# Optimization experiments

Hardware: AMD Instinct MI355X
Metric: run time of the kernel (lower is better)

Reference implementation:

```python
import jax, jax.numpy as jnp
import numpy as np

N = 40000; E = 640000; F_IN = 128; HID = 32; HEADS = 4; G = 64
NEG_SLOPE = 0.2; LN_EPS = 1e-5


def setup_inputs() -> dict:
    key = jax.random.key(0)
    ks = jax.random.split(key, 24)
    rn = lambda k, shape, s=0.1: jax.random.normal(k, shape, jnp.float32) * s
    d = {}
    d["x"] = jax.random.normal(ks[0], (N, F_IN), jnp.float32)
    d["edge_index"] = jax.random.randint(ks[1], (2, E), 0, N)
    d["batch"] = jnp.sort(jax.random.randint(ks[2], (N,), 0, G))
    # GAT layer 0: in F_IN -> HID per head, HEADS heads, concat
    d["W0"] = rn(ks[3], (F_IN, HEADS * HID))
    d["as0"] = rn(ks[4], (HEADS, HID)); d["ad0"] = rn(ks[5], (HEADS, HID))
    d["b0"] = jnp.zeros((HEADS * HID,), jnp.float32)
    d["ln0_g"] = jnp.ones((HEADS * HID,), jnp.float32); d["ln0_b"] = jnp.zeros((HEADS * HID,), jnp.float32)
    # GAT layer 1: HEADS*HID -> HID per head, HEADS heads, concat
    d["W1"] = rn(ks[6], (HEADS * HID, HEADS * HID))
    d["as1"] = rn(ks[7], (HEADS, HID)); d["ad1"] = rn(ks[8], (HEADS, HID))
    d["b1"] = jnp.zeros((HEADS * HID,), jnp.float32)
    d["ln1_g"] = jnp.ones((HEADS * HID,), jnp.float32); d["ln1_b"] = jnp.zeros((HEADS * HID,), jnp.float32)
    # GAT layer 2: HEADS*HID -> HID, 1 head, no concat
    d["W2"] = rn(ks[9], (HEADS * HID, HID))
    d["as2"] = rn(ks[10], (1, HID)); d["ad2"] = rn(ks[11], (1, HID))
    d["b2"] = jnp.zeros((HID,), jnp.float32)
    d["ln2_g"] = jnp.ones((HID,), jnp.float32); d["ln2_b"] = jnp.zeros((HID,), jnp.float32)
    # classifier: HID -> HID//2 -> 2
    d["fc1_w"] = rn(ks[12], (HID, HID // 2)); d["fc1_b"] = jnp.zeros((HID // 2,), jnp.float32)
    d["fc2_w"] = rn(ks[13], (HID // 2, 2)); d["fc2_b"] = jnp.zeros((2,), jnp.float32)
    return d


def gat_layer(x, src, dst, W, a_s, a_d, b, heads, out_c, concat):
    n = x.shape[0]
    h = (x @ W).reshape(n, heads, out_c)            # [N,H,C]
    al_s = jnp.sum(h * a_s, axis=-1)                # [N,H]
    al_d = jnp.sum(h * a_d, axis=-1)                # [N,H]
    e = jax.nn.leaky_relu(al_s[src] + al_d[dst], NEG_SLOPE)  # [E,H]
    m = jax.ops.segment_max(e, dst, num_segments=n)          # segment softmax over dst
    ex = jnp.exp(e - m[dst])
    s = jax.ops.segment_sum(ex, dst, num_segments=n)
    alpha = ex / (s[dst] + 1e-16)                   # [E,H]
    out = jax.ops.segment_sum(h[src] * alpha[:, :, None], dst, num_segments=n)  # [N,H,C]
    out = out.reshape(n, heads * out_c) if concat else out.mean(axis=1)
    return out + b


def layer_norm(x, g, b):
    mu = x.mean(-1, keepdims=True)
    var = jnp.var(x, axis=-1, keepdims=True)
    return (x - mu) * jax.lax.rsqrt(var + LN_EPS) * g + b


def reference(x, edge_index, batch, W0, as0, ad0, b0, ln0_g, ln0_b, W1, as1, ad1, b1, ln1_g, ln1_b, W2, as2, ad2, b2, ln2_g, ln2_b, fc1_w, fc1_b, fc2_w, fc2_b):
    src, dst = edge_index[0], edge_index[1]
    h = gat_layer(x, src, dst, W0, as0, ad0, b0, HEADS, HID, True)
    h = jax.nn.elu(layer_norm(h, ln0_g, ln0_b))
    h = gat_layer(h, src, dst, W1, as1, ad1, b1, HEADS, HID, True)
    h = jax.nn.elu(layer_norm(h, ln1_g, ln1_b))
    h = gat_layer(h, src, dst, W2, as2, ad2, b2, 1, HID, False)
    h = jax.nn.elu(layer_norm(h, ln2_g, ln2_b))
    cnt = jax.ops.segment_sum(jnp.ones((h.shape[0],), h.dtype), batch, num_segments=G)
    hg = jax.ops.segment_sum(h, batch, num_segments=G) / jnp.maximum(cnt, 1.0)[:, None]  # global mean pool [G,HID]
    z = jax.nn.relu(hg @ fc1_w + fc1_b)
    return z @ fc2_w + fc2_b
```

## Files before the change

kernel.cpp:

```cpp
#include <hip/hip_runtime.h>
#include <hip/hip_fp16.h>
#include <math.h>

#define NN 40000
#define EE 640000
#define NG 64
#define SCAN_BLOCKS ((NN + 1023) / 1024)

__device__ __forceinline__ float eluf(float x) { return x > 0.f ? x : expm1f(x); }

typedef const __attribute__((address_space(1))) char gas_char;
typedef __attribute__((address_space(3))) char las_char;

__device__ __forceinline__ void async_copy16(void* l, const void* g) {
  __builtin_amdgcn_global_load_lds((gas_char*)g, (las_char*)l, 16, 0, 0);
}

typedef __fp16 f16x2 __attribute__((ext_vector_type(2)));
__device__ __forceinline__ unsigned packh(float lo, float hi) {
  f16x2 p = __builtin_amdgcn_cvt_pkrtz(lo, hi);
  union { f16x2 h; unsigned u; } c; c.h = p; return c.u;
}
__device__ __forceinline__ float hlo(unsigned p) {
  union { unsigned u; f16x2 h; } c; c.u = p; return (float)c.h.x;
}
__device__ __forceinline__ float hhi(unsigned p) {
  union { unsigned u; f16x2 h; } c; c.u = p; return (float)c.h.y;
}

__global__ void zero_int_kernel(int* __restrict__ p, int n) {
  int i = blockIdx.x * 256 + threadIdx.x;
  if (i < n) p[i] = 0;
}

__global__ void count_deg_kernel(const int* __restrict__ dst, int* __restrict__ deg, int e) {
  int i = blockIdx.x * 256 + threadIdx.x;
  if (i < e) atomicAdd(&deg[dst[i]], 1);
}

__global__ __launch_bounds__(1024) void scanA_kernel(const int* __restrict__ deg,
                                                     int* __restrict__ row_ptr,
                                                     int* __restrict__ bsum, int n) {
  __shared__ int wsum[16];
  int t = threadIdx.x, lane = t & 63, wid = t >> 6;
  int i = blockIdx.x * 1024 + t;
  int v = (i < n) ? deg[i] : 0;
#pragma unroll
  for (int off = 1; off < 64; off <<= 1) {
    int u = __shfl_up(v, off);
    if (lane >= off) v += u;
  }
  if (lane == 63) wsum[wid] = v;
  __syncthreads();
  if (t < 16) {
    int w = wsum[t];
#pragma unroll
    for (int off = 1; off < 16; off <<= 1) {
      int u = __shfl_up(w, off);
      if (t >= off) w += u;
    }
    wsum[t] = w;
  }
  __syncthreads();
  if (wid > 0) v += wsum[wid - 1];
  if (i < n) row_ptr[i + 1] = v;
  if (t == 1023) bsum[blockIdx.x] = v;
}

__global__ void scanB_kernel(const int* __restrict__ bsum, int* __restrict__ boff, int nb) {
  int lane = threadIdx.x;
  int v = (lane < nb) ? bsum[lane] : 0;
  int orig = v;
#pragma unroll
  for (int off = 1; off < 64; off <<= 1) {
    int u = __shfl_up(v, off);
    if (lane >= off) v += u;
  }
  if (lane < nb) boff[lane] = v - orig;
}

__global__ __launch_bounds__(1024) void scanC_kernel(int* __restrict__ row_ptr,
                                                     const int* __restrict__ boff,
                                                     int* __restrict__ cursor, int n) {
  int i = blockIdx.x * 1024 + threadIdx.x;
  if (i < n) {
    int v = row_ptr[i + 1] + boff[i >> 10];
    row_ptr[i + 1] = v;
    if (i + 1 < n) cursor[i + 1] = v;
    if (i == 0) { cursor[0] = 0; row_ptr[0] = 0; }
  }
}

__global__ void scatter_kernel(const int* __restrict__ src, const int* __restrict__ dst,
                               int* __restrict__ cursor, int* __restrict__ csr_src, int e) {
  int i = blockIdx.x * 256 + threadIdx.x;
  if (i < e) {
    int d = dst[i];
    int pos = atomicAdd(&cursor[d], 1);
    csr_src[pos] = src[i];
  }
}

__global__ __launch_bounds__(256, 3) void gemm128_kernel(
    const float* __restrict__ x, const float* __restrict__ W,
    const float* __restrict__ a_s, const float* __restrict__ a_d,
    unsigned* __restrict__ hb, float* __restrict__ als, float* __restrict__ ald)
{
  __shared__ float xs[2][64 * 32];
  __shared__ float ws[2][32 * 128];

  int t = threadIdx.x;
  int row0 = blockIdx.x * 64;
  const char* xgb = (const char*)x + (size_t)row0 * 512;

  {
    int li0 = t, li1 = t + 256;
    async_copy16((char*)xs[0] + li0 * 16, xgb + (li0 >> 3) * 512 + (li0 & 7) * 16);
    async_copy16((char*)xs[0] + li1 * 16, xgb + (li1 >> 3) * 512 + (li1 & 7) * 16);
    const char* wg = (const char*)W;
#pragma unroll
    for (int p = 0; p < 4; ++p)
      async_copy16((char*)ws[0] + p * 4096 + t * 16, wg + p * 4096 + t * 16);
  }
  __syncthreads();

  int cg = t & 31, rg = t >> 5;
  int r0 = rg * 8;
  int jlo = 2 * cg;

  float acc[8][4];
#pragma unroll
  for (int r = 0; r < 8; ++r)
#pragma unroll
    for (int c = 0; c < 4; ++c) acc[r][c] = 0.f;

  for (int ch = 0; ch < 4; ++ch) {
    if (ch < 3) {
      int b = (ch + 1) & 1;
      int li0 = t, li1 = t + 256;
      const char* xg = xgb + (ch + 1) * 128;
      async_copy16((char*)xs[b] + li0 * 16, xg + (li0 >> 3) * 512 + (li0 & 7) * 16);
      async_copy16((char*)xs[b] + li1 * 16, xg + (li1 >> 3) * 512 + (li1 & 7) * 16);
      const char* wg = (const char*)W + (size_t)(ch + 1) * 32 * 128 * 4;
#pragma unroll
      for (int p = 0; p < 4; ++p)
        async_copy16((char*)ws[b] + p * 4096 + t * 16, wg + p * 4096 + t * 16);
    }
    const float* wc = ws[ch & 1];
    const float* xc = xs[ch & 1];
#pragma unroll
    for (int kk = 0; kk < 32; kk += 4) {
      float2 wlo[4], whi[4];
#pragma unroll
      for (int q = 0; q < 4; ++q) {
        wlo[q] = *reinterpret_cast<const float2*>(&wc[(kk + q) * 128 + jlo]);
        whi[q] = *reinterpret_cast<const float2*>(&wc[(kk + q) * 128 + 64 + jlo]);
      }
#pragma unroll
      for (int r = 0; r < 8; ++r) {
        float4 xv = *reinterpret_cast<const float4*>(&xc[(r0 + r) * 32 + kk]);
        float a0 = acc[r][0], a1 = acc[r][1], a2 = acc[r][2], a3 = acc[r][3];
        a0 = fmaf(xv.x, wlo[0].x, a0); a1 = fmaf(xv.x, wlo[0].y, a1);
        a2 = fmaf(xv.x, whi[0].x, a2); a3 = fmaf(xv.x, whi[0].y, a3);
        a0 = fmaf(xv.y, wlo[1].x, a0); a1 = fmaf(xv.y, wlo[1].y, a1);
        a2 = fmaf(xv.y, whi[1].x, a2); a3 = fmaf(xv.y, whi[1].y, a3);
        a0 = fmaf(xv.z, wlo[2].x, a0); a1 = fmaf(xv.z, wlo[2].y, a1);
        a2 = fmaf(xv.z, whi[2].x, a2); a3 = fmaf(xv.z, whi[2].y, a3);
        a0 = fmaf(xv.w, wlo[3].x, a0); a1 = fmaf(xv.w, wlo[3].y, a1);
        a2 = fmaf(xv.w, whi[3].x, a2); a3 = fmaf(xv.w, whi[3].y, a3);
        acc[r][0] = a0; acc[r][1] = a1; acc[r][2] = a2; acc[r][3] = a3;
      }
    }
    __syncthreads();
  }

#pragma unroll
  for (int r = 0; r < 8; ++r) {
    uint2 pv;
    pv.x = packh(acc[r][0], acc[r][2]);
    pv.y = packh(acc[r][1], acc[r][3]);
    *reinterpret_cast<uint2*>(&hb[(size_t)(row0 + r0 + r) * 64 + jlo]) = pv;
  }

  float as0 = a_s[jlo], as1 = a_s[jlo + 1], as2 = a_s[jlo + 64], as3 = a_s[jlo + 65];
  float ad0 = a_d[jlo], ad1 = a_d[jlo + 1], ad2 = a_d[jlo + 64], ad3 = a_d[jlo + 65];
  int lane = t & 63;
#pragma unroll
  for (int r = 0; r < 8; ++r) {
    float psa = fmaf(acc[r][0], as0, acc[r][1] * as1);
    float psb = fmaf(acc[r][2], as2, acc[r][3] * as3);
    float pda = fmaf(acc[r][0], ad0, acc[r][1] * ad1);
    float pdb = fmaf(acc[r][2], ad2, acc[r][3] * ad3);
#pragma unroll
    for (int m = 1; m < 16; m <<= 1) {
      psa += __shfl_xor(psa, m); psb += __shfl_xor(psb, m);
      pda += __shfl_xor(pda, m); pdb += __shfl_xor(pdb, m);
    }
    if ((lane & 15) == 0) {
      int hA = (lane >> 4) & 1;
      size_t row = (size_t)(row0 + r0 + r);
      als[row * 4 + hA] = psa; als[row * 4 + hA + 2] = psb;
      ald[row * 4 + hA] = pda; ald[row * 4 + hA + 2] = pdb;
    }
  }
}

__global__ __launch_bounds__(256, 2) void gemm32_kernel(
    const float* __restrict__ x, const float* __restrict__ W,
    const float* __restrict__ a_s, const float* __restrict__ a_d,
    float* __restrict__ h, float* __restrict__ als, float* __restrict__ ald)
{
  __shared__ float xs[64 * 128];
  __shared__ float ws[2][32 * 32];
  int t = threadIdx.x;
  int row0 = blockIdx.x * 64;
  {
    const char* xg = (const char*)(x + (size_t)row0 * 128);
    char* xl = (char*)xs;
#pragma unroll
    for (int it = 0; it < 8; ++it)
      async_copy16(xl + it * 4096 + t * 16, xg + it * 4096 + t * 16);
  }
  async_copy16((char*)ws[0] + t * 16, (const char*)W + t * 16);
  __syncthreads();

  int cg = t & 7, rg = t >> 3;
  int r0 = rg * 2, c0 = cg * 4;
  float acc[2][4];
#pragma unroll
  for (int r = 0; r < 2; ++r)
#pragma unroll
    for (int c = 0; c < 4; ++c) acc[r][c] = 0.f;

  for (int ch = 0; ch < 4; ++ch) {
    if (ch < 3) {
      const char* wg = (const char*)W + (size_t)(ch + 1) * 32 * 32 * 4;
      async_copy16((char*)ws[(ch + 1) & 1] + t * 16, wg + t * 16);
    }
    const float* wc = ws[ch & 1];
    const float* xc = xs + ch * 32;
#pragma unroll
    for (int kk = 0; kk < 32; kk += 4) {
      float4 wv[4];
#pragma unroll
      for (int q = 0; q < 4; ++q)
        wv[q] = *reinterpret_cast<const float4*>(&wc[(kk + q) * 32 + c0]);
#pragma unroll
      for (int r = 0; r < 2; ++r) {
        float4 xv = *reinterpret_cast<const float4*>(&xc[(r0 + r) * 128 + kk]);
#pragma unroll
        for (int c = 0; c < 4; ++c) {
          float a = acc[r][c];
          a = fmaf(xv.x, (&wv[0].x)[c], a);
          a = fmaf(xv.y, (&wv[1].x)[c], a);
          a = fmaf(xv.z, (&wv[2].x)[c], a);
          a = fmaf(xv.w, (&wv[3].x)[c], a);
          acc[r][c] = a;
        }
      }
    }
    __syncthreads();
  }

#pragma unroll
  for (int r = 0; r < 2; ++r) {
    float4 hv = make_float4(acc[r][0], acc[r][1], acc[r][2], acc[r][3]);
    *reinterpret_cast<float4*>(&h[(size_t)(row0 + r0 + r) * 32 + c0]) = hv;
  }
  float asv[4], adv[4];
#pragma unroll
  for (int c = 0; c < 4; ++c) { asv[c] = a_s[c0 + c]; adv[c] = a_d[c0 + c]; }
#pragma unroll
  for (int r = 0; r < 2; ++r) {
    float ps = acc[r][0] * asv[0] + acc[r][1] * asv[1] + acc[r][2] * asv[2] + acc[r][3] * asv[3];
    float pd = acc[r][0] * adv[0] + acc[r][1] * adv[1] + acc[r][2] * adv[2] + acc[r][3] * adv[3];
#pragma unroll
    for (int m = 1; m < 8; m <<= 1) { ps += __shfl_xor(ps, m); pd += __shfl_xor(pd, m); }
    if ((t & 7) == 0) {
      als[row0 + r0 + r] = ps;
      ald[row0 + r0 + r] = pd;
    }
  }
}

__global__ __launch_bounds__(256) void aggregate128_kernel(
    const unsigned* __restrict__ hb, const float* __restrict__ als, const float* __restrict__ ald,
    const int* __restrict__ row_ptr, const int* __restrict__ csr_src,
    const float* __restrict__ bias, const float* __restrict__ ln_g, const float* __restrict__ ln_b,
    float* __restrict__ out, int n)
{
  __shared__ int s_src[4][64];
  __shared__ float2 s_w[4][64][2];
  int t = threadIdx.x, lane = t & 63, wid = t >> 6;
  int node = blockIdx.x * 4 + wid;
  if (node >= n) return;
  int start = row_ptr[node], end = row_ptr[node + 1];
  int deg = end - start;

  float4 adq = reinterpret_cast<const float4*>(ald)[node];
  float adl[4] = {adq.x, adq.y, adq.z, adq.w};
  int hi = lane >> 5, c = lane & 31;
  int hsel = c >> 4;
  float a0 = 0.f, a1 = 0.f, a2 = 0.f, a3 = 0.f;
  float ssum0 = 0.f, ssum1 = 0.f;

  if (deg <= 64) {
    int s = 0;
    if (lane < deg) s = csr_src[start + lane];
    float4 q = reinterpret_cast<const float4*>(als)[s];
    float v[4] = {q.x, q.y, q.z, q.w};
    float ex[4];
#pragma unroll
    for (int hh = 0; hh < 4; ++hh) {
      float w = v[hh] + adl[hh];
      w = w > 0.f ? w : 0.2f * w;
      ex[hh] = __expf(w);
    }
    s_src[wid][lane] = s;
    s_w[wid][lane][0] = make_float2(ex[0], ex[2]);
    s_w[wid][lane][1] = make_float2(ex[1], ex[3]);

    int d1 = deg >> 1, d0c = deg - d1;
    int base = hi ? d0c : 0;
    int cnt = hi ? d1 : d0c;
    float b0a = 0.f, b1a = 0.f, b2a = 0.f, b3a = 0.f;
    float sb0 = 0.f, sb1 = 0.f;
    int j = 0;
    for (; j + 2 <= cnt; j += 2) {
      int sa = s_src[wid][base + j];
      int sb = s_src[wid][base + j + 1];
      uint2 ua = *reinterpret_cast<const uint2*>(&hb[(size_t)sa * 64 + 2 * c]);
      uint2 ub = *reinterpret_cast<const uint2*>(&hb[(size_t)sb * 64 + 2 * c]);
      float2 wa = s_w[wid][base + j][hsel];
      float2 wb = s_w[wid][base + j + 1][hsel];
      a0 = fmaf(wa.x, hlo(ua.x), a0); a1 = fmaf(wa.x, hlo(ua.y), a1);
      a2 = fmaf(wa.y, hhi(ua.x), a2); a3 = fmaf(wa.y, hhi(ua.y), a3);
      ssum0 += wa.x; ssum1 += wa.y;
      b0a = fmaf(wb.x, hlo(ub.x), b0a); b1a = fmaf(wb.x, hlo(ub.y), b1a);
      b2a = fmaf(wb.y, hhi(ub.x), b2a); b3a = fmaf(wb.y, hhi(ub.y), b3a);
      sb0 += wb.x; sb1 += wb.y;
    }
    if (j < cnt) {
      int sa = s_src[wid][base + j];
      uint2 ua = *reinterpret_cast<const uint2*>(&hb[(size_t)sa * 64 + 2 * c]);
      float2 wa = s_w[wid][base + j][hsel];
      a0 = fmaf(wa.x, hlo(ua.x), a0); a1 = fmaf(wa.x, hlo(ua.y), a1);
      a2 = fmaf(wa.y, hhi(ua.x), a2); a3 = fmaf(wa.y, hhi(ua.y), a3);
      ssum0 += wa.x; ssum1 += wa.y;
    }
    a0 += b0a; a1 += b1a; a2 += b2a; a3 += b3a;
    ssum0 += sb0; ssum1 += sb1;
    a0 += __shfl_xor(a0, 32); a1 += __shfl_xor(a1, 32);
    a2 += __shfl_xor(a2, 32); a3 += __shfl_xor(a3, 32);
    ssum0 += __shfl_xor(ssum0, 32); ssum1 += __shfl_xor(ssum1, 32);
  } else {
    for (int eb = start; eb < end; eb += 64) {
      int e = eb + lane;
      int s = 0;
      float exv[4] = {0.f, 0.f, 0.f, 0.f};
      if (e < end) {
        s = csr_src[e];
        float4 q = reinterpret_cast<const float4*>(als)[s];
        float av[4] = {q.x, q.y, q.z, q.w};
#pragma unroll
        for (int hh = 0; hh < 4; ++hh) {
          float v = av[hh] + adl[hh];
          v = v > 0.f ? v : 0.2f * v;
          exv[hh] = __expf(v);
        }
      }
      s_src[wid][lane] = s;
      s_w[wid][lane][0] = make_float2(exv[0], exv[2]);
      s_w[wid][lane][1] = make_float2(exv[1], exv[3]);
      int cnt = end - eb; if (cnt > 64) cnt = 64;
      for (int j = 0; j < cnt; ++j) {
        int sj = s_src[wid][j];
        uint2 u = *reinterpret_cast<const uint2*>(&hb[(size_t)sj * 64 + 2 * c]);
        float2 w = s_w[wid][j][hsel];
        a0 = fmaf(w.x, hlo(u.x), a0); a1 = fmaf(w.x, hlo(u.y), a1);
        a2 = fmaf(w.y, hhi(u.x), a2); a3 = fmaf(w.y, hhi(u.y), a3);
        ssum0 += w.x; ssum1 += w.y;
      }
    }
    a0 *= 0.5f; a1 *= 0.5f; a2 *= 0.5f; a3 *= 0.5f;
    ssum0 *= 0.5f; ssum1 *= 0.5f;
    a0 += __shfl_xor(a0, 32); a1 += __shfl_xor(a1, 32);
    a2 += __shfl_xor(a2, 32); a3 += __shfl_xor(a3, 32);
    ssum0 += __shfl_xor(ssum0, 32); ssum1 += __shfl_xor(ssum1, 32);
  }

  float2 blo = *reinterpret_cast<const float2*>(&bias[2 * c]);
  float2 bhi = *reinterpret_cast<const float2*>(&bias[2 * c + 64]);
  float is0 = 1.f / (ssum0 + 1e-16f), is1 = 1.f / (ssum1 + 1e-16f);
  float o0 = a0 * is0 + blo.x;
  float o1 = a1 * is0 + blo.y;
  float o2 = a2 * is1 + bhi.x;
  float o3 = a3 * is1 + bhi.y;
  float red = o0 + o1 + o2 + o3;
  float sq2 = o0 * o0 + o1 * o1 + o2 * o2 + o3 * o3;
#pragma unroll
  for (int m = 1; m < 64; m <<= 1) {
    red += __shfl_xor(red, m);
    sq2 += __shfl_xor(sq2, m);
  }
  float mu = red * (1.f / 256.f);
  float var = sq2 * (1.f / 256.f) - mu * mu;
  float rstd = rsqrtf(var + 1e-5f);
  int f = 2 * c + 64 * hi;
  float2 gv = *reinterpret_cast<const float2*>(&ln_g[f]);
  float2 bv = *reinterpret_cast<const float2*>(&ln_b[f]);
  float dx = (hi ? o2 : o0) - mu, dy = (hi ? o3 : o1) - mu;
  float2 yv;
  yv.x = eluf(dx * rstd * gv.x + bv.x);
  yv.y = eluf(dy * rstd * gv.y + bv.y);
  *reinterpret_cast<float2*>(&out[(size_t)node * 128 + f]) = yv;
}

__global__ __launch_bounds__(256) void aggregate32_kernel(
    const float* __restrict__ h, const float* __restrict__ als, const float* __restrict__ ald,
    const int* __restrict__ row_ptr, const int* __restrict__ csr_src,
    const float* __restrict__ bias, const float* __restrict__ ln_g, const float* __restrict__ ln_b,
    float* __restrict__ out, int n)
{
  __shared__ int s_src[4][64];
  __shared__ float s_ex[4][64];
  int t = threadIdx.x, lane = t & 63, wid = t >> 6;
  int node = blockIdx.x * 4 + wid;
  if (node >= n) return;
  int start = row_ptr[node], end = row_ptr[node + 1];
  int deg = end - start;
  float adl = ald[node];
  int hi = lane >> 5, col = lane & 31;
  float acc0 = 0.f, ssum = 0.f;

  if (deg <= 64) {
    int s = 0;
    if (lane < deg) s = csr_src[start + lane];
    float v = als[s] + adl;
    v = v > 0.f ? v : 0.2f * v;
    float ex = __expf(v);
    s_src[wid][lane] = s;
    s_ex[wid][lane] = ex;

    int d1 = deg >> 1, d0c = deg - d1;
    int base = hi ? d0c : 0;
    int cnt = hi ? d1 : d0c;
    float acc1 = 0.f, ssum1 = 0.f;
    int j = 0;
    for (; j + 2 <= cnt; j += 2) {
      int sa = s_src[wid][base + j];
      int sb = s_src[wid][base + j + 1];
      float ha = h[(size_t)sa * 32 + col];
      float hbv = h[(size_t)sb * 32 + col];
      float wa = s_ex[wid][base + j];
      float wb = s_ex[wid][base + j + 1];
      acc0 = fmaf(wa, ha, acc0); ssum += wa;
      acc1 = fmaf(wb, hbv, acc1); ssum1 += wb;
    }
    if (j < cnt) {
      float wa = s_ex[wid][base + j];
      acc0 = fmaf(wa, h[(size_t)s_src[wid][base + j] * 32 + col], acc0);
      ssum += wa;
    }
    acc0 += acc1; ssum += ssum1;
    acc0 += __shfl_xor(acc0, 32);
    ssum += __shfl_xor(ssum, 32);
  } else {
    for (int eb = start; eb < end; eb += 64) {
      int e = eb + lane;
      int s = 0; float ex = 0.f;
      if (e < end) {
        s = csr_src[e];
        float v = als[s] + adl;
        v = v > 0.f ? v : 0.2f * v;
        ex = __expf(v);
      }
      s_src[wid][lane] = s;
      s_ex[wid][lane] = ex;
      int cnt = end - eb; if (cnt > 64) cnt = 64;
      for (int j = 0; j < cnt; ++j) {
        float w = s_ex[wid][j];
        acc0 = fmaf(w, h[(size_t)s_src[wid][j] * 32 + col], acc0);
        ssum += w;
      }
    }
    acc0 *= 0.5f; ssum *= 0.5f;
    acc0 += __shfl_xor(acc0, 32);
    ssum += __shfl_xor(ssum, 32);
  }

  float o0 = acc0 / (ssum + 1e-16f) + bias[col];
  float red = o0, sq2 = o0 * o0;
#pragma unroll
  for (int m = 1; m < 64; m <<= 1) {
    red += __shfl_xor(red, m);
    sq2 += __shfl_xor(sq2, m);
  }
  float mu = red * (1.f / 64.f);
  float var = sq2 * (1.f / 64.f) - mu * mu;
  float rstd = rsqrtf(var + 1e-5f);
  float y0 = (o0 - mu) * rstd * ln_g[col] + ln_b[col];
  if (lane < 32) out[(size_t)node * 32 + col] = eluf(y0);
}

__device__ __forceinline__ int lower_bound_dev(const int* a, int n, int key) {
  int lo = 0, hi = n;
  while (lo < hi) { int mid = (lo + hi) >> 1; if (a[mid] < key) lo = mid + 1; else hi = mid; }
  return lo;
}

__global__ __launch_bounds__(256) void poolfc_kernel(
    const float* __restrict__ x2, const int* __restrict__ batch,
    const float* __restrict__ fc1w, const float* __restrict__ fc1b,
    const float* __restrict__ fc2w, const float* __restrict__ fc2b,
    float* __restrict__ out, int n)
{
  int g = blockIdx.x;
  int lo = lower_bound_dev(batch, n, g);
  int hi = lower_bound_dev(batch, n, g + 1);
  int t = threadIdx.x;
  int c = t & 31, r = t >> 5;
  float acc = 0.f;
  for (int i = lo + r; i < hi; i += 8) acc += x2[(size_t)i * 32 + c];
  __shared__ float red[8][32];
  __shared__ float hgl[32];
  __shared__ float zl[16];
  red[r][c] = acc;
  __syncthreads();
  if (r == 0) {
    float s = 0.f;
#pragma unroll
    for (int k = 0; k < 8; ++k) s += red[k][c];
    float cnt = (float)(hi - lo);
    hgl[c] = s / fmaxf(cnt, 1.f);
  }
  __syncthreads();
  if (t < 16) {
    float a = fc1b[t];
#pragma unroll
    for (int k = 0; k < 32; ++k) a = fmaf(hgl[k], fc1w[k * 16 + t], a);
    zl[t] = fmaxf(a, 0.f);
  }
  __syncthreads();
  if (t < 2) {
    float a = fc2b[t];
#pragma unroll
    for (int j = 0; j < 16; ++j) a = fmaf(zl[j], fc2w[j * 2 + t], a);
    out[g * 2 + t] = a;
  }
}

extern "C" void kernel_launch(void* const* d_in, const int* in_sizes, int n_in,
                              void* d_out, int out_size, void* d_ws, size_t ws_size,
                              hipStream_t stream) {
  const float* x    = (const float*)d_in[0];
  const int*   ei   = (const int*)d_in[1];
  const int*   batch= (const int*)d_in[2];
  const float* W0   = (const float*)d_in[3];
  const float* as0  = (const float*)d_in[4];
  const float* ad0  = (const float*)d_in[5];
  const float* b0   = (const float*)d_in[6];
  const float* ln0g = (const float*)d_in[7];
  const float* ln0b = (const float*)d_in[8];
  const float* W1   = (const float*)d_in[9];
  const float* as1  = (const float*)d_in[10];
  const float* ad1  = (const float*)d_in[11];
  const float* b1   = (const float*)d_in[12];
  const float* ln1g = (const float*)d_in[13];
  const float* ln1b = (const float*)d_in[14];
  const float* W2   = (const float*)d_in[15];
  const float* as2  = (const float*)d_in[16];
  const float* ad2  = (const float*)d_in[17];
  const float* b2   = (const float*)d_in[18];
  const float* ln2g = (const float*)d_in[19];
  const float* ln2b = (const float*)d_in[20];
  const float* fc1w = (const float*)d_in[21];
  const float* fc1b = (const float*)d_in[22];
  const float* fc2w = (const float*)d_in[23];
  const float* fc2b = (const float*)d_in[24];
  float* out = (float*)d_out;

  const int* srce = ei;
  const int* dste = ei + EE;

  unsigned* hb = (unsigned*)d_ws;
  float* B2  = (float*)(hb + (size_t)NN * 64);
  float* als = B2 + (size_t)NN * 128;
  float* ald = als + (size_t)NN * 4;
  float* h2  = ald + (size_t)NN * 4;
  float* x2  = h2 + (size_t)NN * 32;
  int* deg      = (int*)(x2 + (size_t)NN * 32);
  int* row_ptr  = deg + NN;
  int* cursor   = row_ptr + NN + 1;
  int* csr_src  = cursor + NN;
  int* bsum     = csr_src + EE;
  int* boff     = bsum + SCAN_BLOCKS;

  zero_int_kernel<<<(NN + 255) / 256, 256, 0, stream>>>(deg, NN);
  count_deg_kernel<<<(EE + 255) / 256, 256, 0, stream>>>(dste, deg, EE);
  scanA_kernel<<<SCAN_BLOCKS, 1024, 0, stream>>>(deg, row_ptr, bsum, NN);
  scanB_kernel<<<1, 64, 0, stream>>>(bsum, boff, SCAN_BLOCKS);
  scanC_kernel<<<SCAN_BLOCKS, 1024, 0, stream>>>(row_ptr, boff, cursor, NN);
  scatter_kernel<<<(EE + 255) / 256, 256, 0, stream>>>(srce, dste, cursor, csr_src, EE);

  gemm128_kernel<<<625, 256, 0, stream>>>(x, W0, as0, ad0, hb, als, ald);
  aggregate128_kernel<<<(NN + 3) / 4, 256, 0, stream>>>(hb, als, ald, row_ptr, csr_src,
                                                        b0, ln0g, ln0b, B2, NN);
  gemm128_kernel<<<625, 256, 0, stream>>>(B2, W1, as1, ad1, hb, als, ald);
  aggregate128_kernel<<<(NN + 3) / 4, 256, 0, stream>>>(hb, als, ald, row_ptr, csr_src,
                                                        b1, ln1g, ln1b, B2, NN);
  gemm32_kernel<<<625, 256, 0, stream>>>(B2, W2, as2, ad2, h2, als, ald);
  aggregate32_kernel<<<(NN + 3) / 4, 256, 0, stream>>>(h2, als, ald, row_ptr, csr_src,
                                                       b2, ln2g, ln2b, x2, NN);
  poolfc_kernel<<<NG, 256, 0, stream>>>(x2, batch, fc1w, fc1b, fc2w, fc2b, out, NN);
}
```

Before: 270.0 us.

## Assign one node per half-wavefront in aggregation and fuse scan block-offset pass

The aggregation kernels now map each node to a 32-lane half-wavefront instead of a full 64-lane wavefront, so each wave handles two nodes. Each half-wave processes all of its node's edges, which removes the cross-half shuffle reduction and shortens the layer-norm shuffle tree. The intent is better lane utilisation, since the average degree of about 16 left many lanes idle. Separately, the single-block scanB kernel is removed and each scanC block computes its own offset by summing the preceding block sums, saving one launch. The new launch grids rely on N being divisible by 8 and drop the node bounds check.

```diff
diff --git a/kernel.cpp b/kernel.cpp
--- a/kernel.cpp
+++ b/kernel.cpp
@@ -67,24 +67,23 @@
   if (t == 1023) bsum[blockIdx.x] = v;
 }
 
-__global__ void scanB_kernel(const int* __restrict__ bsum, int* __restrict__ boff, int nb) {
-  int lane = threadIdx.x;
-  int v = (lane < nb) ? bsum[lane] : 0;
-  int orig = v;
-#pragma unroll
-  for (int off = 1; off < 64; off <<= 1) {
-    int u = __shfl_up(v, off);
-    if (lane >= off) v += u;
-  }
-  if (lane < nb) boff[lane] = v - orig;
-}
-
 __global__ __launch_bounds__(1024) void scanC_kernel(int* __restrict__ row_ptr,
-                                                     const int* __restrict__ boff,
+                                                     const int* __restrict__ bsum,
                                                      int* __restrict__ cursor, int n) {
-  int i = blockIdx.x * 1024 + threadIdx.x;
+  __shared__ int off_s;
+  int t = threadIdx.x;
+  int b = blockIdx.x;
+  if (t < 64) {
+    int v = (t < b && t < SCAN_BLOCKS) ? bsum[t] : 0;
+#pragma unroll
+    for (int m = 1; m < 64; m <<= 1) v += __shfl_xor(v, m);
+    if (t == 0) off_s = v;
+  }
+  __syncthreads();
+  int off = off_s;
+  int i = b * 1024 + t;
   if (i < n) {
-    int v = row_ptr[i + 1] + boff[i >> 10];
+    int v = row_ptr[i + 1] + off;
     row_ptr[i + 1] = v;
     if (i + 1 < n) cursor[i + 1] = v;
     if (i == 0) { cursor[0] = 0; row_ptr[0] = 0; }
@@ -289,50 +288,44 @@
     const float* __restrict__ bias, const float* __restrict__ ln_g, const float* __restrict__ ln_b,
     float* __restrict__ out, int n)
 {
-  __shared__ int s_src[4][64];
-  __shared__ float2 s_w[4][64][2];
+  __shared__ int s_src[4][2][32];
+  __shared__ float2 s_w[4][2][32][2];
   int t = threadIdx.x, lane = t & 63, wid = t >> 6;
-  int node = blockIdx.x * 4 + wid;
-  if (node >= n) return;
+  int hw = lane >> 5, c = lane & 31;
+  int node = blockIdx.x * 8 + wid * 2 + hw;
   int start = row_ptr[node], end = row_ptr[node + 1];
   int deg = end - start;
 
   float4 adq = reinterpret_cast<const float4*>(ald)[node];
-  float adl[4] = {adq.x, adq.y, adq.z, adq.w};
-  int hi = lane >> 5, c = lane & 31;
   int hsel = c >> 4;
   float a0 = 0.f, a1 = 0.f, a2 = 0.f, a3 = 0.f;
   float ssum0 = 0.f, ssum1 = 0.f;
 
-  if (deg <= 64) {
+  if (deg <= 32) {
     int s = 0;
-    if (lane < deg) s = csr_src[start + lane];
-    float4 q = reinterpret_cast<const float4*>(als)[s];
-    float v[4] = {q.x, q.y, q.z, q.w};
-    float ex[4];
-#pragma unroll
-    for (int hh = 0; hh < 4; ++hh) {
-      float w = v[hh] + adl[hh];
-      w = w > 0.f ? w : 0.2f * w;
-      ex[hh] = __expf(w);
-    }
-    s_src[wid][lane] = s;
-    s_w[wid][lane][0] = make_float2(ex[0], ex[2]);
-    s_w[wid][lane][1] = make_float2(ex[1], ex[3]);
-
-    int d1 = deg >> 1, d0c = deg - d1;
-    int base = hi ? d0c : 0;
-    int cnt = hi ? d1 : d0c;
+    float ex0 = 0.f, ex1 = 0.f, ex2 = 0.f, ex3 = 0.f;
+    if (c < deg) {
+      s = csr_src[start + c];
+      float4 q = reinterpret_cast<const float4*>(als)[s];
+      float v0 = q.x + adq.x, v1 = q.y + adq.y, v2 = q.z + adq.z, v3 = q.w + adq.w;
+      v0 = v0 > 0.f ? v0 : 0.2f * v0; v1 = v1 > 0.f ? v1 : 0.2f * v1;
+      v2 = v2 > 0.f ? v2 : 0.2f * v2; v3 = v3 > 0.f ? v3 : 0.2f * v3;
+      ex0 = __expf(v0); ex1 = __expf(v1); ex2 = __expf(v2); ex3 = __expf(v3);
+    }
+    s_src[wid][hw][c] = s;
+    s_w[wid][hw][c][0] = make_float2(ex0, ex2);
+    s_w[wid][hw][c][1] = make_float2(ex1, ex3);
+
     float b0a = 0.f, b1a = 0.f, b2a = 0.f, b3a = 0.f;
     float sb0 = 0.f, sb1 = 0.f;
     int j = 0;
-    for (; j + 2 <= cnt; j += 2) {
-      int sa = s_src[wid][base + j];
-      int sb = s_src[wid][base + j + 1];
+    for (; j + 2 <= deg; j += 2) {
+      int sa = s_src[wid][hw][j];
+      int sb = s_src[wid][hw][j + 1];
       uint2 ua = *reinterpret_cast<const uint2*>(&hb[(size_t)sa * 64 + 2 * c]);
       uint2 ub = *reinterpret_cast<const uint2*>(&hb[(size_t)sb * 64 + 2 * c]);
-      float2 wa = s_w[wid][base + j][hsel];
-      float2 wb = s_w[wid][base + j + 1][hsel];
+      float2 wa = s_w[wid][hw][j][hsel];
+      float2 wb = s_w[wid][hw][j + 1][hsel];
       a0 = fmaf(wa.x, hlo(ua.x), a0); a1 = fmaf(wa.x, hlo(ua.y), a1);
       a2 = fmaf(wa.y, hhi(ua.x), a2); a3 = fmaf(wa.y, hhi(ua.y), a3);
       ssum0 += wa.x; ssum1 += wa.y;
@@ -340,53 +333,41 @@
       b2a = fmaf(wb.y, hhi(ub.x), b2a); b3a = fmaf(wb.y, hhi(ub.y), b3a);
       sb0 += wb.x; sb1 += wb.y;
     }
-    if (j < cnt) {
-      int sa = s_src[wid][base + j];
+    if (j < deg) {
+      int sa = s_src[wid][hw][j];
       uint2 ua = *reinterpret_cast<const uint2*>(&hb[(size_t)sa * 64 + 2 * c]);
-      float2 wa = s_w[wid][base + j][hsel];
+      float2 wa = s_w[wid][hw][j][hsel];
       a0 = fmaf(wa.x, hlo(ua.x), a0); a1 = fmaf(wa.x, hlo(ua.y), a1);
       a2 = fmaf(wa.y, hhi(ua.x), a2); a3 = fmaf(wa.y, hhi(ua.y), a3);
       ssum0 += wa.x; ssum1 += wa.y;
     }
     a0 += b0a; a1 += b1a; a2 += b2a; a3 += b3a;
     ssum0 += sb0; ssum1 += sb1;
-    a0 += __shfl_xor(a0, 32); a1 += __shfl_xor(a1, 32);
-    a2 += __shfl_xor(a2, 32); a3 += __shfl_xor(a3, 32);
-    ssum0 += __shfl_xor(ssum0, 32); ssum1 += __shfl_xor(ssum1, 32);
   } else {
-    for (int eb = start; eb < end; eb += 64) {
-      int e = eb + lane;
+    for (int eb = 0; eb < deg; eb += 32) {
       int s = 0;
-      float exv[4] = {0.f, 0.f, 0.f, 0.f};
-      if (e < end) {
-        s = csr_src[e];
+      float ex0 = 0.f, ex1 = 0.f, ex2 = 0.f, ex3 = 0.f;
+      if (eb + c < deg) {
+        s = csr_src[start + eb + c];
         float4 q = reinterpret_cast<const float4*>(als)[s];
-        float av[4] = {q.x, q.y, q.z, q.w};
-#pragma unroll
-        for (int hh = 0; hh < 4; ++hh) {
-          float v = av[hh] + adl[hh];
-          v = v > 0.f ? v : 0.2f * v;
-          exv[hh] = __expf(v);
-        }
-      }
-      s_src[wid][lane] = s;
-      s_w[wid][lane][0] = make_float2(exv[0], exv[2]);
-      s_w[wid][lane][1] = make_float2(exv[1], exv[3]);
-      int cnt = end - eb; if (cnt > 64) cnt = 64;
+        float v0 = q.x + adq.x, v1 = q.y + adq.y, v2 = q.z + adq.z, v3 = q.w + adq.w;
+        v0 = v0 > 0.f ? v0 : 0.2f * v0; v1 = v1 > 0.f ? v1 : 0.2f * v1;
+        v2 = v2 > 0.f ? v2 : 0.2f * v2; v3 = v3 > 0.f ? v3 : 0.2f * v3;
+        ex0 = __expf(v0); ex1 = __expf(v1); ex2 = __expf(v2); ex3 = __expf(v3);
+      }
+      s_src[wid][hw][c] = s;
+      s_w[wid][hw][c][0] = make_float2(ex0, ex2);
+      s_w[wid][hw][c][1] = make_float2(ex1, ex3);
+      int cnt = deg - eb; if (cnt > 32) cnt = 32;
       for (int j = 0; j < cnt; ++j) {
-        int sj = s_src[wid][j];
+        int sj = s_src[wid][hw][j];
         uint2 u = *reinterpret_cast<const uint2*>(&hb[(size_t)sj * 64 + 2 * c]);
-        float2 w = s_w[wid][j][hsel];
+        float2 w = s_w[wid][hw][j][hsel];
         a0 = fmaf(w.x, hlo(u.x), a0); a1 = fmaf(w.x, hlo(u.y), a1);
         a2 = fmaf(w.y, hhi(u.x), a2); a3 = fmaf(w.y, hhi(u.y), a3);
         ssum0 += w.x; ssum1 += w.y;
       }
     }
-    a0 *= 0.5f; a1 *= 0.5f; a2 *= 0.5f; a3 *= 0.5f;
-    ssum0 *= 0.5f; ssum1 *= 0.5f;
-    a0 += __shfl_xor(a0, 32); a1 += __shfl_xor(a1, 32);
-    a2 += __shfl_xor(a2, 32); a3 += __shfl_xor(a3, 32);
-    ssum0 += __shfl_xor(ssum0, 32); ssum1 += __shfl_xor(ssum1, 32);
   }
 
   float2 blo = *reinterpret_cast<const float2*>(&bias[2 * c]);
@@ -399,21 +380,24 @@
   float red = o0 + o1 + o2 + o3;
   float sq2 = o0 * o0 + o1 * o1 + o2 * o2 + o3 * o3;
 #pragma unroll
-  for (int m = 1; m < 64; m <<= 1) {
+  for (int m = 1; m < 32; m <<= 1) {
     red += __shfl_xor(red, m);
     sq2 += __shfl_xor(sq2, m);
   }
-  float mu = red * (1.f / 256.f);
-  float var = sq2 * (1.f / 256.f) - mu * mu;
+  float mu = red * (1.f / 128.f);
+  float var = sq2 * (1.f / 128.f) - mu * mu;
   float rstd = rsqrtf(var + 1e-5f);
-  int f = 2 * c + 64 * hi;
-  float2 gv = *reinterpret_cast<const float2*>(&ln_g[f]);
-  float2 bv = *reinterpret_cast<const float2*>(&ln_b[f]);
-  float dx = (hi ? o2 : o0) - mu, dy = (hi ? o3 : o1) - mu;
-  float2 yv;
-  yv.x = eluf(dx * rstd * gv.x + bv.x);
-  yv.y = eluf(dy * rstd * gv.y + bv.y);
-  *reinterpret_cast<float2*>(&out[(size_t)node * 128 + f]) = yv;
+  float2 glo = *reinterpret_cast<const float2*>(&ln_g[2 * c]);
+  float2 ghi = *reinterpret_cast<const float2*>(&ln_g[2 * c + 64]);
+  float2 bl2 = *reinterpret_cast<const float2*>(&ln_b[2 * c]);
+  float2 bh2 = *reinterpret_cast<const float2*>(&ln_b[2 * c + 64]);
+  float2 ylo, yhi;
+  ylo.x = eluf((o0 - mu) * rstd * glo.x + bl2.x);
+  ylo.y = eluf((o1 - mu) * rstd * glo.y + bl2.y);
+  yhi.x = eluf((o2 - mu) * rstd * ghi.x + bh2.x);
+  yhi.y = eluf((o3 - mu) * rstd * ghi.y + bh2.y);
+  *reinterpret_cast<float2*>(&out[(size_t)node * 128 + 2 * c]) = ylo;
+  *reinterpret_cast<float2*>(&out[(size_t)node * 128 + 64 + 2 * c]) = yhi;
 }
 
 __global__ __launch_bounds__(256) void aggregate32_kernel(
@@ -422,85 +406,77 @@
     const float* __restrict__ bias, const float* __restrict__ ln_g, const float* __restrict__ ln_b,
     float* __restrict__ out, int n)
 {
-  __shared__ int s_src[4][64];
-  __shared__ float s_ex[4][64];
+  __shared__ int s_src[4][2][32];
+  __shared__ float s_ex[4][2][32];
   int t = threadIdx.x, lane = t & 63, wid = t >> 6;
-  int node = blockIdx.x * 4 + wid;
-  if (node >= n) return;
+  int hw = lane >> 5, c = lane & 31;
+  int node = blockIdx.x * 8 + wid * 2 + hw;
   int start = row_ptr[node], end = row_ptr[node + 1];
   int deg = end - start;
   float adl = ald[node];
-  int hi = lane >> 5, col = lane & 31;
   float acc0 = 0.f, ssum = 0.f;
 
-  if (deg <= 64) {
-    int s = 0;
-    if (lane < deg) s = csr_src[start + lane];
-    float v = als[s] + adl;
-    v = v > 0.f ? v : 0.2f * v;
-    float ex = __expf(v);
-    s_src[wid][lane] = s;
-    s_ex[wid][lane] = ex;
-
-    int d1 = deg >> 1, d0c = deg - d1;
-    int base = hi ? d0c : 0;
-    int cnt = hi ? d1 : d0c;
+  if (deg <= 32) {
+    int s = 0; float ex = 0.f;
+    if (c < deg) {
+      s = csr_src[start + c];
+      float v = als[s] + adl;
+      v = v > 0.f ? v : 0.2f * v;
+      ex = __expf(v);
+    }
+    s_src[wid][hw][c] = s;
+    s_ex[wid][hw][c] = ex;
+
     float acc1 = 0.f, ssum1 = 0.f;
     int j = 0;
-    for (; j + 2 <= cnt; j += 2) {
-      int sa = s_src[wid][base + j];
-      int sb = s_src[wid][base + j + 1];
-      float ha = h[(size_t)sa * 32 + col];
-      float hbv = h[(size_t)sb * 32 + col];
-      float wa = s_ex[wid][base + j];
-      float wb = s_ex[wid][base + j + 1];
+    for (; j + 2 <= deg; j += 2) {
+      int sa = s_src[wid][hw][j];
+      int sb = s_src[wid][hw][j + 1];
+      float ha = h[(size_t)sa * 32 + c];
+      float hbv = h[(size_t)sb * 32 + c];
+      float wa = s_ex[wid][hw][j];
+      float wb = s_ex[wid][hw][j + 1];
       acc0 = fmaf(wa, ha, acc0); ssum += wa;
       acc1 = fmaf(wb, hbv, acc1); ssum1 += wb;
     }
-    if (j < cnt) {
-      float wa = s_ex[wid][base + j];
-      acc0 = fmaf(wa, h[(size_t)s_src[wid][base + j] * 32 + col], acc0);
+    if (j < deg) {
+      float wa = s_ex[wid][hw][j];
+      acc0 = fmaf(wa, h[(size_t)s_src[wid][hw][j] * 32 + c], acc0);
       ssum += wa;
     }
     acc0 += acc1; ssum += ssum1;
-    acc0 += __shfl_xor(acc0, 32);
-    ssum += __shfl_xor(ssum, 32);
   } else {
-    for (int eb = start; eb < end; eb += 64) {
-      int e = eb + lane;
+    for (int eb = 0; eb < deg; eb += 32) {
       int s = 0; float ex = 0.f;
-      if (e < end) {
-        s = csr_src[e];
+      if (eb + c < deg) {
+        s = csr_src[start + eb + c];
         float v = als[s] + adl;
         v = v > 0.f ? v : 0.2f * v;
         ex = __expf(v);
       }
-      s_src[wid][lane] = s;
-      s_ex[wid][lane] = ex;
-      int cnt = end - eb; if (cnt > 64) cnt = 64;
+      s_src[wid][hw][c] = s;
+      s_ex[wid][hw][c] = ex;
+      int cnt = deg - eb; if (cnt > 32) cnt = 32;
       for (int j = 0; j < cnt; ++j) {
-        float w = s_ex[wid][j];
-        acc0 = fmaf(w, h[(size_t)s_src[wid][j] * 32 + col], acc0);
+        float w = s_ex[wid][hw][j];
+        acc0 = fmaf(w, h[(size_t)s_src[wid][hw][j] * 32 + c], acc0);
         ssum += w;
       }
     }
-    acc0 *= 0.5f; ssum *= 0.5f;
-    acc0 += __shfl_xor(acc0, 32);
-    ssum += __shfl_xor(ssum, 32);
-  }
-
-  float o0 = acc0 / (ssum + 1e-16f) + bias[col];
+  }
+
+  float o0 = acc0 / (ssum + 1e-16f) + bias[c];
   float red = o0, sq2 = o0 * o0;
 #pragma unroll
-  for (int m = 1; m < 64; m <<= 1) {
+  for (int m = 1; m < 32; m <<= 1) {
     red += __shfl_xor(red, m);
     sq2 += __shfl_xor(sq2, m);
   }
-  float mu = red * (1.f / 64.f);
-  float var = sq2 * (1.f / 64.f) - mu * mu;
+  float mu = red * (1.f / 32.f);
+  float var = sq2 * (1.f / 32.f) - mu * mu;
   float rstd = rsqrtf(var + 1e-5f);
-  float y0 = (o0 - mu) * rstd * ln_g[col] + ln_b[col];
-  if (lane < 32) out[(size_t)node * 32 + col] = eluf(y0);
+  float y0 = (o0 - mu) * rstd * ln_g[c] + ln_b[c];
+  out[(size_t)node * 32 + c] = eluf(y0);
 }
 
 __device__ __forceinline__ int lower_bound_dev(const int* a, int n, int key) {
@@ -594,23 +570,21 @@
   int* cursor   = row_ptr + NN + 1;
   int* csr_src  = cursor + NN;
   int* bsum     = csr_src + EE;
-  int* boff     = bsum + SCAN_BLOCKS;
 
   zero_int_kernel<<<(NN + 255) / 256, 256, 0, stream>>>(deg, NN);
   count_deg_kernel<<<(EE + 255) / 256, 256, 0, stream>>>(dste, deg, EE);
   scanA_kernel<<<SCAN_BLOCKS, 1024, 0, stream>>>(deg, row_ptr, bsum, NN);
-  scanB_kernel<<<1, 64, 0, stream>>>(bsum, boff, SCAN_BLOCKS);
-  scanC_kernel<<<SCAN_BLOCKS, 1024, 0, stream>>>(row_ptr, boff, cursor, NN);
+  scanC_kernel<<<SCAN_BLOCKS, 1024, 0, stream>>>(row_ptr, bsum, cursor, NN);
   scatter_kernel<<<(EE + 255) / 256, 256, 0, stream>>>(srce, dste, cursor, csr_src, EE);
 
   gemm128_kernel<<<625, 256, 0, stream>>>(x, W0, as0, ad0, hb, als, ald);
-  aggregate128_kernel<<<(NN + 3) / 4, 256, 0, stream>>>(hb, als, ald, row_ptr, csr_src,
-                                                        b0, ln0g, ln0b, B2, NN);
+  aggregate128_kernel<<<NN / 8, 256, 0, stream>>>(hb, als, ald, row_ptr, csr_src,
+                                                  b0, ln0g, ln0b, B2, NN);
   gemm128_kernel<<<625, 256, 0, stream>>>(B2, W1, as1, ad1, hb, als, ald);
-  aggregate128_kernel<<<(NN + 3) / 4, 256, 0, stream>>>(hb, als, ald, row_ptr, csr_src,
-                                                        b1, ln1g, ln1b, B2, NN);
+  aggregate128_kernel<<<NN / 8, 256, 0, stream>>>(hb, als, ald, row_ptr, csr_src,
+                                                  b1, ln1g, ln1b, B2, NN);
   gemm32_kernel<<<625, 256, 0, stream>>>(B2, W2, as2, ad2, h2, als, ald);
-  aggregate32_kernel<<<(NN + 3) / 4, 256, 0, stream>>>(h2, als, ald, row_ptr, csr_src,
-                                                       b2, ln2g, ln2b, x2, NN);
+  aggregate32_kernel<<<NN / 8, 256, 0, stream>>>(h2, als, ald, row_ptr, csr_src,
+                                                 b2, ln2g, ln2b, x2, NN);
   poolfc_kernel<<<NG, 256, 0, stream>>>(x2, batch, fc1w, fc1b, fc2w, fc2b, out, NN);
 }
```

After: 255.1 us. -5.5%, faster.
